# Kernel optimization log

Measured on AMD Instinct MI355X. Metric: run time of the kernel, lower is better.

The kernel has to match this reference:

```python
import jax, jax.numpy as jnp
import numpy as np

D_MODEL = 512
NUM_HEADS = 8
D_HEAD = D_MODEL // NUM_HEADS
B, S = 2, 4096


def setup_inputs() -> dict:
    key = jax.random.key(0)
    ks = jax.random.split(key, 9)
    scale = 1.0 / np.sqrt(D_MODEL)
    x = jax.random.normal(ks[0], (B, S, D_MODEL), dtype=jnp.float32)
    Wq = jax.random.normal(ks[1], (D_MODEL, D_MODEL), dtype=jnp.float32) * scale
    Wk = jax.random.normal(ks[2], (D_MODEL, D_MODEL), dtype=jnp.float32) * scale
    Wv = jax.random.normal(ks[3], (D_MODEL, D_MODEL), dtype=jnp.float32) * scale
    Wo = jax.random.normal(ks[4], (D_MODEL, D_MODEL), dtype=jnp.float32) * scale
    bq = jnp.zeros((D_MODEL,), jnp.float32)
    bk = jnp.zeros((D_MODEL,), jnp.float32)
    bv = jnp.zeros((D_MODEL,), jnp.float32)
    bo = jnp.zeros((D_MODEL,), jnp.float32)
    return {"x": x, "Wq": Wq, "bq": bq, "Wk": Wk, "bk": bk,
            "Wv": Wv, "bv": bv, "Wo": Wo, "bo": bo}


def _split_heads(t):
    # [B, S, D] -> [B, H, S, d_head]
    b, s, _ = t.shape
    return t.reshape(b, s, NUM_HEADS, D_HEAD).transpose(0, 2, 1, 3)


def reference(x, Wq, bq, Wk, bk, Wv, bv, Wo, bo):
    q = _split_heads(x @ Wq + bq)  # [B,H,S,dh]
    k = _split_heads(x @ Wk + bk)
    v = _split_heads(x @ Wv + bv)
    scores = jnp.einsum("bhqd,bhkd->bhqk", q, k) / jnp.sqrt(
        jnp.asarray(D_HEAD, x.dtype))
    attn = jax.nn.softmax(scores, axis=-1)  # dropout is identity at inference
    out = jnp.einsum("bhqk,bhkd->bhqd", attn, v)  # [B,H,S,dh]
    out = out.transpose(0, 2, 1, 3).reshape(x.shape[0], x.shape[1], D_MODEL)
    return out @ Wo + bo
```

## Files before the change

### kernel.cpp

```cpp
#include <hip/hip_runtime.h>
#include <cstddef>

#define NB   2
#define SEQ  4096
#define DM   512
#define NH   8
#define DH   64
#define MTOT 8192
#define KSPLIT 2
#define KSEQ (SEQ / KSPLIT)

#define QSCALE 0.18033688011112042f

typedef __attribute__((ext_vector_type(8))) short short8;
typedef __attribute__((ext_vector_type(4))) float f32x4;

__device__ __forceinline__ ushort f2bf(float f) {
  unsigned u = __builtin_bit_cast(unsigned, f);
  u += 0x7FFFu + ((u >> 16) & 1u);
  return (ushort)(u >> 16);
}
__device__ __forceinline__ float bf2f(ushort b) {
  return __builtin_bit_cast(float, ((unsigned)b) << 16);
}
__device__ __forceinline__ unsigned cvt_pk_bf16(float lo, float hi) {
  unsigned r;
  asm("v_cvt_pk_bf16_f32 %0, %1, %2" : "=v"(r) : "v"(lo), "v"(hi));
  return r;
}
__device__ __forceinline__ float fexp2(float x) {
#if __has_builtin(__builtin_amdgcn_exp2f)
  return __builtin_amdgcn_exp2f(x);
#else
  float r;
  asm("v_exp_f32 %0, %1" : "=v"(r) : "v"(x));
  return r;
#endif
}

__global__ __launch_bounds__(256)
void xcast_k(const float* __restrict__ x, ushort* __restrict__ xb) {
  const int i = (blockIdx.x * 256 + threadIdx.x) * 8;
  float4 a = *(const float4*)(x + i);
  float4 b = *(const float4*)(x + i + 4);
  ushort h[8] = {f2bf(a.x), f2bf(a.y), f2bf(a.z), f2bf(a.w),
                 f2bf(b.x), f2bf(b.y), f2bf(b.z), f2bf(b.w)};
  *(uint4*)(xb + i) = *(const uint4*)h;
}

__global__ __launch_bounds__(256)
void prep_w_k(const float* __restrict__ Wq, const float* __restrict__ Wk,
              const float* __restrict__ Wv, const float* __restrict__ Wo,
              ushort* __restrict__ WTq, ushort* __restrict__ WTk,
              ushort* __restrict__ WTv, ushort* __restrict__ WTh,
              ushort* __restrict__ WTl) {
  const int z = blockIdx.z;
  const float* W = (z == 0) ? Wq : (z == 1) ? Wk : (z == 2) ? Wv : Wo;
  ushort* WT = (z == 0) ? WTq : (z == 1) ? WTk : (z == 2) ? WTv : WTh;
  ushort* WTlo = (z == 3) ? WTl : nullptr;

  __shared__ float t[32][33];
  const int k0 = blockIdx.x * 32, n0 = blockIdx.y * 32;
  const int tx = threadIdx.x & 31, ty = threadIdx.x >> 5;
#pragma unroll
  for (int i = 0; i < 32; i += 8)
    t[ty + i][tx] = W[(size_t)(k0 + ty + i) * DM + n0 + tx];
  __syncthreads();
#pragma unroll
  for (int i = 0; i < 32; i += 8) {
    float v = t[tx][ty + i];
    ushort h = f2bf(v);
    WT[(size_t)(n0 + ty + i) * DM + k0 + tx] = h;
    if (WTlo) WTlo[(size_t)(n0 + ty + i) * DM + k0 + tx] = f2bf(v - bf2f(h));
  }
}

__global__ __launch_bounds__(256)
void qkv_gemm_k(const ushort* __restrict__ xb,
                const ushort* __restrict__ WTq, const ushort* __restrict__ WTk,
                const ushort* __restrict__ WTv,
                const float* __restrict__ bq, const float* __restrict__ bk,
                const float* __restrict__ bv,
                ushort* __restrict__ Qb, ushort* __restrict__ Kb,
                ushort* __restrict__ Vb) {
  __shared__ ushort smem[17408];
  ushort (*As)[40] = (ushort(*)[40])smem;
  ushort (*Bs)[40] = (ushort(*)[40])(smem + 5120);

  const int z = blockIdx.z;
  const ushort* WT = (z == 0) ? WTq : (z == 1) ? WTk : WTv;
  const float* bias = (z == 0) ? bq : (z == 1) ? bk : bv;
  ushort* outp = (z == 0) ? Qb : (z == 1) ? Kb : Vb;
  const float oscale = (z == 0) ? QSCALE : 1.0f;

  const int tid = threadIdx.x;
  const int w = tid >> 6, l = tid & 63;
  const int g = l >> 4, l15 = l & 15;
  const int wm = w >> 1, wn = w & 1;
  const int m0 = blockIdx.x * 128;
  const int n0 = blockIdx.y * 128;

  const int ar = tid >> 1, ac = (tid & 1) * 16;
  const ushort* Ag = xb + (size_t)(m0 + ar) * DM + ac;
  const ushort* Bg = WT + (size_t)(n0 + ar) * DM + ac;

  uint4 ra0 = *(const uint4*)(Ag);
  uint4 ra1 = *(const uint4*)(Ag + 8);
  uint4 rb0 = *(const uint4*)(Bg);
  uint4 rb1 = *(const uint4*)(Bg + 8);

  float bfn[4];
#pragma unroll
  for (int fn = 0; fn < 4; ++fn)
    bfn[fn] = bias[n0 + wn * 64 + fn * 16 + l15];

  f32x4 acc[4][4];
#pragma unroll
  for (int fm = 0; fm < 4; ++fm)
#pragma unroll
    for (int fn = 0; fn < 4; ++fn) acc[fm][fn] = (f32x4){0.f, 0.f, 0.f, 0.f};

  for (int k0 = 0; k0 < DM; k0 += 32) {
    __syncthreads();
    *(uint4*)&As[ar][ac]     = ra0;
    *(uint4*)&As[ar][ac + 8] = ra1;
    *(uint4*)&Bs[ar][ac]     = rb0;
    *(uint4*)&Bs[ar][ac + 8] = rb1;
    __syncthreads();
    if (k0 + 32 < DM) {
      ra0 = *(const uint4*)(Ag + k0 + 32);
      ra1 = *(const uint4*)(Ag + k0 + 40);
      rb0 = *(const uint4*)(Bg + k0 + 32);
      rb1 = *(const uint4*)(Bg + k0 + 40);
    }
    short8 af[4], bf[4];
#pragma unroll
    for (int fm = 0; fm < 4; ++fm)
      af[fm] = *(const short8*)&As[wm * 64 + fm * 16 + l15][g * 8];
#pragma unroll
    for (int fn = 0; fn < 4; ++fn)
      bf[fn] = *(const short8*)&Bs[wn * 64 + fn * 16 + l15][g * 8];
#pragma unroll
    for (int fm = 0; fm < 4; ++fm)
#pragma unroll
      for (int fn = 0; fn < 4; ++fn)
        acc[fm][fn] = __builtin_amdgcn_mfma_f32_16x16x32_bf16(
            af[fm], bf[fn], acc[fm][fn], 0, 0, 0);
  }

  if (z != 2) {
#pragma unroll
    for (int fm = 0; fm < 4; ++fm)
#pragma unroll
      for (int fn = 0; fn < 4; ++fn)
#pragma unroll
        for (int r = 0; r < 4; ++r) {
          int m = m0 + wm * 64 + fm * 16 + g * 4 + r;
          int n = n0 + wn * 64 + fn * 16 + l15;
          float v = (acc[fm][fn][r] + bfn[fn]) * oscale;
          int b = m >> 12, s = m & (SEQ - 1);
          int h = n >> 6, d = n & 63;
          outp[(size_t)((b * NH + h) * SEQ + s) * DH + d] = f2bf(v);
        }
  } else {
    __syncthreads();
    ushort (*T)[136] = (ushort(*)[136])smem;
#pragma unroll
    for (int fm = 0; fm < 4; ++fm)
#pragma unroll
      for (int fn = 0; fn < 4; ++fn)
#pragma unroll
        for (int r = 0; r < 4; ++r) {
          int ml = wm * 64 + fm * 16 + g * 4 + r;
          int nl = wn * 64 + fn * 16 + l15;
          T[nl][ml] = f2bf(acc[fm][fn][r] + bfn[fn]);
        }
    __syncthreads();
    const int b = m0 >> 12, s0 = m0 & (SEQ - 1);
#pragma unroll
    for (int it = 0; it < 8; ++it) {
      int ch = tid + 256 * it;
      int row = ch >> 4;
      int cc = (ch & 15) * 8;
      int n = n0 + row;
      int h = n >> 6, d = n & 63;
      *(uint4*)&outp[((size_t)(b * NH + h) * DH + d) * SEQ + s0 + cc] =
          *(const uint4*)&T[row][cc];
    }
  }
}

__global__ __launch_bounds__(256)
void combine_k(const float* __restrict__ Po, const float* __restrict__ Dn,
               ushort* __restrict__ Ahb, ushort* __restrict__ Alb) {
  const size_t o = (size_t)(blockIdx.x * 256 + threadIdx.x) * 8;
  const int m = (int)(o >> 9);
  const int c = (int)(o & 511);
  const int b = m >> 12, s = m & (SEQ - 1);
  const int h = c >> 6, d = c & 63;
  const int bh = b * NH + h;
  const size_t i0 = ((size_t)bh * SEQ + s) * DH + d;
  const size_t zoff = (size_t)(NB * NH) * SEQ * DH;
  const float den = Dn[(size_t)bh * SEQ + s] +
                    Dn[(size_t)(NB * NH + bh) * SEQ + s];
  const float inv = __builtin_amdgcn_rcpf(den);
  ushort hh[8], ll[8];
#pragma unroll
  for (int i = 0; i < 8; i += 4) {
    float4 p0 = *(const float4*)(Po + i0 + i);
    float4 p1 = *(const float4*)(Po + zoff + i0 + i);
    float v[4] = {(p0.x + p1.x) * inv, (p0.y + p1.y) * inv,
                  (p0.z + p1.z) * inv, (p0.w + p1.w) * inv};
#pragma unroll
    for (int j = 0; j < 4; ++j) {
      ushort hb = f2bf(v[j]);
      hh[i + j] = hb;
      ll[i + j] = f2bf(v[j] - bf2f(hb));
    }
  }
  *(uint4*)(Ahb + o) = *(const uint4*)hh;
  *(uint4*)(Alb + o) = *(const uint4*)ll;
}

__global__ __launch_bounds__(256)
void oproj_gemm_k(const ushort* __restrict__ Ahb, const ushort* __restrict__ Alb,
                  const ushort* __restrict__ WTh, const ushort* __restrict__ WTl,
                  const float* __restrict__ bo, float* __restrict__ out) {
  __shared__ ushort Ah[128][40];
  __shared__ ushort Al[128][40];
  __shared__ ushort Bh[64][40];
  __shared__ ushort Bl[64][40];

  const int tid = threadIdx.x;
  const int w = tid >> 6, l = tid & 63;
  const int g = l >> 4, l15 = l & 15;
  const int wm = w >> 1, wn = w & 1;
  const int m0 = blockIdx.x * 128;
  const int n0 = blockIdx.y * 64;

  const int ar = tid >> 1, ac = (tid & 1) * 16;
  const int br = tid >> 2, bc = (tid & 3) * 8;

  const ushort* Ahg = Ahb + (size_t)(m0 + ar) * DM + ac;
  const ushort* Alg = Alb + (size_t)(m0 + ar) * DM + ac;
  const ushort* Bhg = WTh + (size_t)(n0 + br) * DM + bc;
  const ushort* Blg = WTl + (size_t)(n0 + br) * DM + bc;

  uint4 rah0 = *(const uint4*)(Ahg);
  uint4 rah1 = *(const uint4*)(Ahg + 8);
  uint4 ral0 = *(const uint4*)(Alg);
  uint4 ral1 = *(const uint4*)(Alg + 8);
  uint4 rbh = *(const uint4*)Bhg;
  uint4 rbl = *(const uint4*)Blg;

  float bfn[2];
#pragma unroll
  for (int fn = 0; fn < 2; ++fn)
    bfn[fn] = bo[n0 + wn * 32 + fn * 16 + l15];

  f32x4 acc[4][2];
#pragma unroll
  for (int fm = 0; fm < 4; ++fm)
#pragma unroll
    for (int fn = 0; fn < 2; ++fn) acc[fm][fn] = (f32x4){0.f, 0.f, 0.f, 0.f};

  for (int k0 = 0; k0 < DM; k0 += 32) {
    __syncthreads();
    *(uint4*)&Ah[ar][ac]     = rah0;
    *(uint4*)&Ah[ar][ac + 8] = rah1;
    *(uint4*)&Al[ar][ac]     = ral0;
    *(uint4*)&Al[ar][ac + 8] = ral1;
    *(uint4*)&Bh[br][bc] = rbh;
    *(uint4*)&Bl[br][bc] = rbl;
    __syncthreads();
    if (k0 + 32 < DM) {
      rah0 = *(const uint4*)(Ahg + k0 + 32);
      rah1 = *(const uint4*)(Ahg + k0 + 40);
      ral0 = *(const uint4*)(Alg + k0 + 32);
      ral1 = *(const uint4*)(Alg + k0 + 40);
      rbh = *(const uint4*)(Bhg + k0 + 32);
      rbl = *(const uint4*)(Blg + k0 + 32);
    }
    short8 ah[4], al[4], bh[2], bl[2];
#pragma unroll
    for (int fm = 0; fm < 4; ++fm) {
      ah[fm] = *(const short8*)&Ah[wm * 64 + fm * 16 + l15][g * 8];
      al[fm] = *(const short8*)&Al[wm * 64 + fm * 16 + l15][g * 8];
    }
#pragma unroll
    for (int fn = 0; fn < 2; ++fn) {
      bh[fn] = *(const short8*)&Bh[wn * 32 + fn * 16 + l15][g * 8];
      bl[fn] = *(const short8*)&Bl[wn * 32 + fn * 16 + l15][g * 8];
    }
#pragma unroll
    for (int fm = 0; fm < 4; ++fm)
#pragma unroll
      for (int fn = 0; fn < 2; ++fn) {
        f32x4 c = acc[fm][fn];
        c = __builtin_amdgcn_mfma_f32_16x16x32_bf16(ah[fm], bh[fn], c, 0, 0, 0);
        c = __builtin_amdgcn_mfma_f32_16x16x32_bf16(ah[fm], bl[fn], c, 0, 0, 0);
        c = __builtin_amdgcn_mfma_f32_16x16x32_bf16(al[fm], bh[fn], c, 0, 0, 0);
        acc[fm][fn] = c;
      }
  }

#pragma unroll
  for (int fm = 0; fm < 4; ++fm)
#pragma unroll
    for (int fn = 0; fn < 2; ++fn)
#pragma unroll
      for (int r = 0; r < 4; ++r) {
        int mm = m0 + wm * 64 + fm * 16 + g * 4 + r;
        int n = n0 + wn * 32 + fn * 16 + l15;
        out[(size_t)mm * DM + n] = acc[fm][fn][r] + bfn[fn];
      }
}

__global__ __launch_bounds__(256, 4)
void attn_mfma_k(const ushort* __restrict__ Q, const ushort* __restrict__ K,
                 const ushort* __restrict__ VT, float* __restrict__ Po,
                 float* __restrict__ Dn) {
  __shared__ ushort Ks[2][64][72];
  __shared__ unsigned Vt[2][64][36];

  const int tid = threadIdx.x;
  const int w   = tid >> 6;
  const int l   = tid & 63;
  const int g   = l >> 4;
  const int l15 = l & 15;
  const int bh  = blockIdx.y;
  const int z   = blockIdx.z;
  const int q0  = blockIdx.x * 128 + w * 32;
  const int tb  = z * KSEQ;

  short8 qb[2][2];
#pragma unroll
  for (int qh = 0; qh < 2; ++qh) {
    const ushort* Qrow = Q + ((size_t)bh * SEQ + q0 + qh * 16 + l15) * DH;
    qb[qh][0] = *(const short8*)(Qrow + g * 8);
    qb[qh][1] = *(const short8*)(Qrow + 32 + g * 8);
  }

  short8 vones;
#pragma unroll
  for (int i = 0; i < 8; ++i) vones[i] = (short)0x3F80;

  f32x4 acc[2][4];
  f32x4 accl[2];
#pragma unroll
  for (int qh = 0; qh < 2; ++qh) {
    accl[qh] = (f32x4){0.f, 0.f, 0.f, 0.f};
#pragma unroll
    for (int dt = 0; dt < 4; ++dt) acc[qh][dt] = (f32x4){0.f, 0.f, 0.f, 0.f};
  }

  const ushort* Kg = K + (size_t)bh * SEQ * DH;

  const int rho  = tid >> 2;
  const int kcol = (tid & 3) * 16;
  const int sig  = 32 * ((rho >> 5) & 1) + 8 * ((rho >> 2) & 3) +
                   4 * ((rho >> 4) & 1) + (rho & 3);
  const ushort* Kp = Kg + (size_t)(tb + sig) * DH + kcol;

  const int vrow = tid >> 2;
  const int vcb  = (tid & 3) * 8;
  const unsigned* Vrow =
      (const unsigned*)(VT + ((size_t)bh * DH + vrow) * SEQ) + tb / 2 + vcb;

  uint4 kr0 = *(const uint4*)(Kp);
  uint4 kr1 = *(const uint4*)(Kp + 8);
  uint4 vv0 = *(const uint4*)(Vrow);
  uint4 vv1 = *(const uint4*)(Vrow + 4);

  int cur = 0;
  for (int t0 = 0; t0 < KSEQ; t0 += 64) {
    *(uint4*)&Ks[cur][rho][kcol]     = kr0;
    *(uint4*)&Ks[cur][rho][kcol + 8] = kr1;
    *(uint4*)&Vt[cur][vrow][vcb]     = vv0;
    *(uint4*)&Vt[cur][vrow][vcb + 4] = vv1;
    if (t0 + 64 < KSEQ) {
      kr0 = *(const uint4*)(Kp + (size_t)(t0 + 64) * DH);
      kr1 = *(const uint4*)(Kp + (size_t)(t0 + 64) * DH + 8);
      vv0 = *(const uint4*)(Vrow + (t0 + 64) / 2);
      vv1 = *(const uint4*)(Vrow + (t0 + 64) / 2 + 4);
    }
    __syncthreads();

    f32x4 s[2][4];
    __builtin_amdgcn_s_setprio(1);
#pragma unroll
    for (int nf = 0; nf < 4; ++nf) {
      short8 ka0 = *(const short8*)&Ks[cur][nf * 16 + l15][g * 8];
      short8 ka1 = *(const short8*)&Ks[cur][nf * 16 + l15][32 + g * 8];
#pragma unroll
      for (int qh = 0; qh < 2; ++qh) {
        f32x4 c = (f32x4){0.f, 0.f, 0.f, 0.f};
        c = __builtin_amdgcn_mfma_f32_16x16x32_bf16(ka0, qb[qh][0], c, 0, 0, 0);
        c = __builtin_amdgcn_mfma_f32_16x16x32_bf16(ka1, qb[qh][1], c, 0, 0, 0);
        s[qh][nf] = c;
      }
    }
    __builtin_amdgcn_s_setprio(0);

    short8 pa[2][2];
#pragma unroll
    for (int qh = 0; qh < 2; ++qh) {
      float p[4][4];
#pragma unroll
      for (int nf = 0; nf < 4; ++nf)
#pragma unroll
        for (int r = 0; r < 4; ++r) p[nf][r] = fexp2(s[qh][nf][r]);
      uint4 u0, u1;
      u0.x = cvt_pk_bf16(p[0][0], p[0][1]);
      u0.y = cvt_pk_bf16(p[0][2], p[0][3]);
      u0.z = cvt_pk_bf16(p[1][0], p[1][1]);
      u0.w = cvt_pk_bf16(p[1][2], p[1][3]);
      u1.x = cvt_pk_bf16(p[2][0], p[2][1]);
      u1.y = cvt_pk_bf16(p[2][2], p[2][3]);
      u1.z = cvt_pk_bf16(p[3][0], p[3][1]);
      u1.w = cvt_pk_bf16(p[3][2], p[3][3]);
      pa[qh][0] = __builtin_bit_cast(short8, u0);
      pa[qh][1] = __builtin_bit_cast(short8, u1);
    }

    __builtin_amdgcn_s_setprio(1);
#pragma unroll
    for (int dt = 0; dt < 4; ++dt) {
      short8 vb0 = *(const short8*)&Vt[cur][dt * 16 + l15][4 * g];
      short8 vb1 = *(const short8*)&Vt[cur][dt * 16 + l15][16 + 4 * g];
#pragma unroll
      for (int qh = 0; qh < 2; ++qh) {
        acc[qh][dt] = __builtin_amdgcn_mfma_f32_16x16x32_bf16(pa[qh][0], vb0,
                                                              acc[qh][dt], 0, 0, 0);
        acc[qh][dt] = __builtin_amdgcn_mfma_f32_16x16x32_bf16(pa[qh][1], vb1,
                                                              acc[qh][dt], 0, 0, 0);
      }
    }
#pragma unroll
    for (int qh = 0; qh < 2; ++qh) {
      accl[qh] = __builtin_amdgcn_mfma_f32_16x16x32_bf16(pa[qh][0], vones,
                                                         accl[qh], 0, 0, 0);
      accl[qh] = __builtin_amdgcn_mfma_f32_16x16x32_bf16(pa[qh][1], vones,
                                                         accl[qh], 0, 0, 0);
    }
    __builtin_amdgcn_s_setprio(0);
    cur ^= 1;
  }

  const int zo = z * (NB * NH) + bh;
#pragma unroll
  for (int qh = 0; qh < 2; ++qh) {
#pragma unroll
    for (int dt = 0; dt < 4; ++dt)
#pragma unroll
      for (int r = 0; r < 4; ++r) {
        int srow = q0 + qh * 16 + g * 4 + r;
        Po[((size_t)zo * SEQ + srow) * DH + dt * 16 + l15] = acc[qh][dt][r];
      }
    if (l15 == 0)
#pragma unroll
      for (int r = 0; r < 4; ++r)
        Dn[(size_t)zo * SEQ + q0 + qh * 16 + g * 4 + r] = accl[qh][r];
  }
}

extern "C" void kernel_launch(void* const* d_in, const int* in_sizes, int n_in,
                              void* d_out, int out_size, void* d_ws, size_t ws_size,
                              hipStream_t stream) {
  const float* x  = (const float*)d_in[0];
  const float* Wq = (const float*)d_in[1];
  const float* bq = (const float*)d_in[2];
  const float* Wk = (const float*)d_in[3];
  const float* bk = (const float*)d_in[4];
  const float* Wv = (const float*)d_in[5];
  const float* bv = (const float*)d_in[6];
  const float* Wo = (const float*)d_in[7];
  const float* bo = (const float*)d_in[8];
  float* out = (float*)d_out;

  const size_t per = (size_t)NB * NH * SEQ * DH;
  const size_t wsz = (size_t)DM * DM;
  ushort* xb  = (ushort*)d_ws;
  ushort* WTq = xb + (size_t)MTOT * DM;
  ushort* WTk = WTq + wsz;
  ushort* WTv = WTk + wsz;
  ushort* WTh = WTv + wsz;
  ushort* WTl = WTh + wsz;
  ushort* Qb  = WTl + wsz;
  ushort* Kb  = Qb + per;
  ushort* Vb  = Kb + per;
  float*  Po  = (float*)(Vb + per);
  float*  Dn  = Po + (size_t)KSPLIT * per;
  ushort* Ahb = xb;
  ushort* Alb = Qb;

  xcast_k<<<MTOT * DM / (256 * 8), 256, 0, stream>>>(x, xb);
  prep_w_k<<<dim3(16, 16, 4), 256, 0, stream>>>(Wq, Wk, Wv, Wo,
                                                WTq, WTk, WTv, WTh, WTl);
  qkv_gemm_k<<<dim3(MTOT / 128, DM / 128, 3), 256, 0, stream>>>(
      xb, WTq, WTk, WTv, bq, bk, bv, Qb, Kb, Vb);
  attn_mfma_k<<<dim3(SEQ / 128, NB * NH, KSPLIT), 256, 0, stream>>>(
      Qb, Kb, Vb, Po, Dn);
  combine_k<<<MTOT * DM / (256 * 8), 256, 0, stream>>>(Po, Dn, Ahb, Alb);
  oproj_gemm_k<<<dim3(MTOT / 128, DM / 64), 256, 0, stream>>>(
      Ahb, Alb, WTh, WTl, bo, out);
}
```

Measured before the change: 141.7 us.

## Merge prep kernels, stage Q/K stores through LDS, widen o-proj tile

Merges the x-cast and weight-transpose kernels into one launch, removing one kernel launch. The Q/K epilogue of the QKV GEMM now writes its tile to shared memory and stores 16-byte coalesced rows per head, replacing scattered 2-byte global writes. The output-projection GEMM tile grows from 128x64 to 128x128, doubling MFMA work per block and reducing A-operand reloads. In exchange it uses more registers and LDS per block and launches half as many o-proj blocks.

Result: no change. 140.2 us (-1.0%).

```diff
diff --git a/kernel.cpp b/kernel.cpp
--- a/kernel.cpp
+++ b/kernel.cpp
@@ -39,28 +39,31 @@
 }
 
 __global__ __launch_bounds__(256)
-void xcast_k(const float* __restrict__ x, ushort* __restrict__ xb) {
-  const int i = (blockIdx.x * 256 + threadIdx.x) * 8;
-  float4 a = *(const float4*)(x + i);
-  float4 b = *(const float4*)(x + i + 4);
-  ushort h[8] = {f2bf(a.x), f2bf(a.y), f2bf(a.z), f2bf(a.w),
-                 f2bf(b.x), f2bf(b.y), f2bf(b.z), f2bf(b.w)};
-  *(uint4*)(xb + i) = *(const uint4*)h;
-}
-
-__global__ __launch_bounds__(256)
-void prep_w_k(const float* __restrict__ Wq, const float* __restrict__ Wk,
-              const float* __restrict__ Wv, const float* __restrict__ Wo,
-              ushort* __restrict__ WTq, ushort* __restrict__ WTk,
-              ushort* __restrict__ WTv, ushort* __restrict__ WTh,
-              ushort* __restrict__ WTl) {
-  const int z = blockIdx.z;
+void prep_all_k(const float* __restrict__ x,
+                const float* __restrict__ Wq, const float* __restrict__ Wk,
+                const float* __restrict__ Wv, const float* __restrict__ Wo,
+                ushort* __restrict__ xb,
+                ushort* __restrict__ WTq, ushort* __restrict__ WTk,
+                ushort* __restrict__ WTv, ushort* __restrict__ WTh,
+                ushort* __restrict__ WTl) {
+  __shared__ float t[32][33];
+  int bid = blockIdx.x;
+  if (bid < 2048) {
+    const int i = (bid * 256 + threadIdx.x) * 8;
+    float4 a = *(const float4*)(x + i);
+    float4 b = *(const float4*)(x + i + 4);
+    ushort h[8] = {f2bf(a.x), f2bf(a.y), f2bf(a.z), f2bf(a.w),
+                   f2bf(b.x), f2bf(b.y), f2bf(b.z), f2bf(b.w)};
+    *(uint4*)(xb + i) = *(const uint4*)h;
+    return;
+  }
+  bid -= 2048;
+  const int z = bid >> 8;
+  const int rr = bid & 255;
   const float* W = (z == 0) ? Wq : (z == 1) ? Wk : (z == 2) ? Wv : Wo;
   ushort* WT = (z == 0) ? WTq : (z == 1) ? WTk : (z == 2) ? WTv : WTh;
   ushort* WTlo = (z == 3) ? WTl : nullptr;
-
-  __shared__ float t[32][33];
-  const int k0 = blockIdx.x * 32, n0 = blockIdx.y * 32;
+  const int k0 = (rr & 15) * 32, n0 = (rr >> 4) * 32;
   const int tx = threadIdx.x & 31, ty = threadIdx.x >> 5;
 #pragma unroll
   for (int i = 0; i < 32; i += 8)
@@ -83,7 +86,7 @@
                 const float* __restrict__ bv,
                 ushort* __restrict__ Qb, ushort* __restrict__ Kb,
                 ushort* __restrict__ Vb) {
-  __shared__ ushort smem[17408];
+  __shared__ ushort smem[17920];
   ushort (*As)[40] = (ushort(*)[40])smem;
   ushort (*Bs)[40] = (ushort(*)[40])(smem + 5120);
 
@@ -148,6 +151,10 @@
             af[fm], bf[fn], acc[fm][fn], 0, 0, 0);
   }
 
+  __syncthreads();
+  ushort (*T)[140] = (ushort(*)[140])smem;
+  const int b = m0 >> 12, s0 = m0 & (SEQ - 1);
+  const int h0 = n0 >> 6;
   if (z != 2) {
 #pragma unroll
     for (int fm = 0; fm < 4; ++fm)
@@ -155,16 +162,21 @@
       for (int fn = 0; fn < 4; ++fn)
 #pragma unroll
         for (int r = 0; r < 4; ++r) {
-          int m = m0 + wm * 64 + fm * 16 + g * 4 + r;
-          int n = n0 + wn * 64 + fn * 16 + l15;
-          float v = (acc[fm][fn][r] + bfn[fn]) * oscale;
-          int b = m >> 12, s = m & (SEQ - 1);
-          int h = n >> 6, d = n & 63;
-          outp[(size_t)((b * NH + h) * SEQ + s) * DH + d] = f2bf(v);
+          int ml = wm * 64 + fm * 16 + g * 4 + r;
+          int nl = wn * 64 + fn * 16 + l15;
+          T[ml][nl] = f2bf((acc[fm][fn][r] + bfn[fn]) * oscale);
         }
+    __syncthreads();
+#pragma unroll
+    for (int it = 0; it < 8; ++it) {
+      int ch = tid + 256 * it;
+      int hl = ch >> 10;
+      int sl = (ch >> 3) & 127;
+      int c8 = (ch & 7) * 8;
+      *(uint4*)(outp + ((size_t)(b * NH + h0 + hl) * SEQ + s0 + sl) * DH + c8) =
+          *(const uint4*)&T[sl][hl * 64 + c8];
+    }
   } else {
-    __syncthreads();
-    ushort (*T)[136] = (ushort(*)[136])smem;
 #pragma unroll
     for (int fm = 0; fm < 4; ++fm)
 #pragma unroll
@@ -176,7 +188,6 @@
           T[nl][ml] = f2bf(acc[fm][fn][r] + bfn[fn]);
         }
     __syncthreads();
-    const int b = m0 >> 12, s0 = m0 & (SEQ - 1);
 #pragma unroll
     for (int it = 0; it < 8; ++it) {
       int ch = tid + 256 * it;
@@ -184,7 +195,7 @@
       int cc = (ch & 15) * 8;
       int n = n0 + row;
       int h = n >> 6, d = n & 63;
-      *(uint4*)&outp[((size_t)(b * NH + h) * DH + d) * SEQ + s0 + cc] =
+      *(uint4*)(outp + ((size_t)(b * NH + h) * DH + d) * SEQ + s0 + cc) =
           *(const uint4*)&T[row][cc];
     }
   }
@@ -228,41 +239,42 @@
                   const float* __restrict__ bo, float* __restrict__ out) {
   __shared__ ushort Ah[128][40];
   __shared__ ushort Al[128][40];
-  __shared__ ushort Bh[64][40];
-  __shared__ ushort Bl[64][40];
+  __shared__ ushort Bh[128][40];
+  __shared__ ushort Bl[128][40];
 
   const int tid = threadIdx.x;
   const int w = tid >> 6, l = tid & 63;
   const int g = l >> 4, l15 = l & 15;
   const int wm = w >> 1, wn = w & 1;
   const int m0 = blockIdx.x * 128;
-  const int n0 = blockIdx.y * 64;
+  const int n0 = blockIdx.y * 128;
 
   const int ar = tid >> 1, ac = (tid & 1) * 16;
-  const int br = tid >> 2, bc = (tid & 3) * 8;
 
   const ushort* Ahg = Ahb + (size_t)(m0 + ar) * DM + ac;
   const ushort* Alg = Alb + (size_t)(m0 + ar) * DM + ac;
-  const ushort* Bhg = WTh + (size_t)(n0 + br) * DM + bc;
-  const ushort* Blg = WTl + (size_t)(n0 + br) * DM + bc;
+  const ushort* Bhg = WTh + (size_t)(n0 + ar) * DM + ac;
+  const ushort* Blg = WTl + (size_t)(n0 + ar) * DM + ac;
 
   uint4 rah0 = *(const uint4*)(Ahg);
   uint4 rah1 = *(const uint4*)(Ahg + 8);
   uint4 ral0 = *(const uint4*)(Alg);
   uint4 ral1 = *(const uint4*)(Alg + 8);
-  uint4 rbh = *(const uint4*)Bhg;
-  uint4 rbl = *(const uint4*)Blg;
-
-  float bfn[2];
-#pragma unroll
-  for (int fn = 0; fn < 2; ++fn)
-    bfn[fn] = bo[n0 + wn * 32 + fn * 16 + l15];
-
-  f32x4 acc[4][2];
+  uint4 rbh0 = *(const uint4*)(Bhg);
+  uint4 rbh1 = *(const uint4*)(Bhg + 8);
+  uint4 rbl0 = *(const uint4*)(Blg);
+  uint4 rbl1 = *(const uint4*)(Blg + 8);
+
+  float bfn[4];
+#pragma unroll
+  for (int fn = 0; fn < 4; ++fn)
+    bfn[fn] = bo[n0 + wn * 64 + fn * 16 + l15];
+
+  f32x4 acc[4][4];
 #pragma unroll
   for (int fm = 0; fm < 4; ++fm)
 #pragma unroll
-    for (int fn = 0; fn < 2; ++fn) acc[fm][fn] = (f32x4){0.f, 0.f, 0.f, 0.f};
+    for (int fn = 0; fn < 4; ++fn) acc[fm][fn] = (f32x4){0.f, 0.f, 0.f, 0.f};
 
   for (int k0 = 0; k0 < DM; k0 += 32) {
     __syncthreads();
@@ -270,32 +282,36 @@
     *(uint4*)&Ah[ar][ac + 8] = rah1;
     *(uint4*)&Al[ar][ac]     = ral0;
     *(uint4*)&Al[ar][ac + 8] = ral1;
-    *(uint4*)&Bh[br][bc] = rbh;
-    *(uint4*)&Bl[br][bc] = rbl;
+    *(uint4*)&Bh[ar][ac]     = rbh0;
+    *(uint4*)&Bh[ar][ac + 8] = rbh1;
+    *(uint4*)&Bl[ar][ac]     = rbl0;
+    *(uint4*)&Bl[ar][ac + 8] = rbl1;
     __syncthreads();
     if (k0 + 32 < DM) {
       rah0 = *(const uint4*)(Ahg + k0 + 32);
       rah1 = *(const uint4*)(Ahg + k0 + 40);
       ral0 = *(const uint4*)(Alg + k0 + 32);
       ral1 = *(const uint4*)(Alg + k0 + 40);
-      rbh = *(const uint4*)(Bhg + k0 + 32);
-      rbl = *(const uint4*)(Blg + k0 + 32);
-    }
-    short8 ah[4], al[4], bh[2], bl[2];
+      rbh0 = *(const uint4*)(Bhg + k0 + 32);
+      rbh1 = *(const uint4*)(Bhg + k0 + 40);
+      rbl0 = *(const uint4*)(Blg + k0 + 32);
+      rbl1 = *(const uint4*)(Blg + k0 + 40);
+    }
+    short8 ah[4], al[4], bh[4], bl[4];
 #pragma unroll
     for (int fm = 0; fm < 4; ++fm) {
       ah[fm] = *(const short8*)&Ah[wm * 64 + fm * 16 + l15][g * 8];
       al[fm] = *(const short8*)&Al[wm * 64 + fm * 16 + l15][g * 8];
     }
 #pragma unroll
-    for (int fn = 0; fn < 2; ++fn) {
-      bh[fn] = *(const short8*)&Bh[wn * 32 + fn * 16 + l15][g * 8];
-      bl[fn] = *(const short8*)&Bl[wn * 32 + fn * 16 + l15][g * 8];
+    for (int fn = 0; fn < 4; ++fn) {
+      bh[fn] = *(const short8*)&Bh[wn * 64 + fn * 16 + l15][g * 8];
+      bl[fn] = *(const short8*)&Bl[wn * 64 + fn * 16 + l15][g * 8];
     }
 #pragma unroll
     for (int fm = 0; fm < 4; ++fm)
 #pragma unroll
-      for (int fn = 0; fn < 2; ++fn) {
+      for (int fn = 0; fn < 4; ++fn) {
         f32x4 c = acc[fm][fn];
         c = __builtin_amdgcn_mfma_f32_16x16x32_bf16(ah[fm], bh[fn], c, 0, 0, 0);
         c = __builtin_amdgcn_mfma_f32_16x16x32_bf16(ah[fm], bl[fn], c, 0, 0, 0);
@@ -307,11 +323,11 @@
 #pragma unroll
   for (int fm = 0; fm < 4; ++fm)
 #pragma unroll
-    for (int fn = 0; fn < 2; ++fn)
+    for (int fn = 0; fn < 4; ++fn)
 #pragma unroll
       for (int r = 0; r < 4; ++r) {
         int mm = m0 + wm * 64 + fm * 16 + g * 4 + r;
-        int n = n0 + wn * 32 + fn * 16 + l15;
+        int n = n0 + wn * 64 + fn * 16 + l15;
         out[(size_t)mm * DM + n] = acc[fm][fn][r] + bfn[fn];
       }
 }
@@ -494,14 +510,13 @@
   ushort* Ahb = xb;
   ushort* Alb = Qb;
 
-  xcast_k<<<MTOT * DM / (256 * 8), 256, 0, stream>>>(x, xb);
-  prep_w_k<<<dim3(16, 16, 4), 256, 0, stream>>>(Wq, Wk, Wv, Wo,
-                                                WTq, WTk, WTv, WTh, WTl);
+  prep_all_k<<<3072, 256, 0, stream>>>(x, Wq, Wk, Wv, Wo, xb,
+                                       WTq, WTk, WTv, WTh, WTl);
   qkv_gemm_k<<<dim3(MTOT / 128, DM / 128, 3), 256, 0, stream>>>(
       xb, WTq, WTk, WTv, bq, bk, bv, Qb, Kb, Vb);
   attn_mfma_k<<<dim3(SEQ / 128, NB * NH, KSPLIT), 256, 0, stream>>>(
       Qb, Kb, Vb, Po, Dn);
   combine_k<<<MTOT * DM / (256 * 8), 256, 0, stream>>>(Po, Dn, Ahb, Alb);
-  oproj_gemm_k<<<dim3(MTOT / 128, DM / 64), 256, 0, stream>>>(
+  oproj_gemm_k<<<dim3(MTOT / 128, DM / 128), 256, 0, stream>>>(
       Ahb, Alb, WTh, WTl, bo, out);
 }
```
